# Performance work log

Measured on AMD Instinct MI355X. Metric: run time of the kernel, lower is better.

## Reference

```python
import jax, jax.numpy as jnp
import numpy as np

EPS = 1e-6
NUM_HEADS = 8
FOCUS = 3.0


def setup_inputs() -> dict:
    key = jax.random.key(0)
    ks = jax.random.split(key, 8)
    B, N, C = 16, 4096, 256
    head_dim, ksz = C // NUM_HEADS, 5
    s = 1.0 / np.sqrt(C)
    return {
        "x": jax.random.normal(ks[0], (B, N, C), jnp.float32),
        "Wq": jax.random.normal(ks[1], (C, C), jnp.float32) * s,
        "Wkv": jax.random.normal(ks[2], (C, 2 * C), jnp.float32) * s,
        "Wp": jax.random.normal(ks[3], (C, C), jnp.float32) * s,
        "bp": jnp.zeros((C,), jnp.float32),
        "scale_param": jnp.zeros((1, 1, C), jnp.float32),
        "pos_enc": jax.random.normal(ks[4], (1, N, C), jnp.float32) * 0.02,
        "dwc_w": jax.random.normal(ks[5], (head_dim, 1, ksz, ksz), jnp.float32) * 0.1,
        "dwc_b": jnp.zeros((head_dim,), jnp.float32),
        "H": 64,
        "W": 64,
    }


def _focus(t, scale, f):
    # relu feature map + power focusing with norm restoration
    t = (jax.nn.relu(t) + EPS) / scale
    tn = jnp.linalg.norm(t, axis=-1, keepdims=True)
    tf = t ** f
    return tf / jnp.linalg.norm(tf, axis=-1, keepdims=True) * tn


def reference(x, Wq, Wkv, Wp, bp, scale_param, pos_enc, dwc_w, dwc_b, H, W):
    B, N, C = x.shape
    h = NUM_HEADS
    d = C // h
    n = N  # sr_ratio == 1

    q = x @ Wq                                  # [B,N,C]
    kv = x @ Wkv                                # [B,N,2C]
    k, v = kv[..., :C], kv[..., C:]
    k = k + pos_enc

    scale = jax.nn.softplus(scale_param)
    q = _focus(q, scale, FOCUS)
    k = _focus(k, scale, FOCUS)

    # split heads: [B,h,N,d]
    qh = q.reshape(B, N, h, d).transpose(0, 2, 1, 3)
    kh = k.reshape(B, n, h, d).transpose(0, 2, 1, 3)
    vh = v.reshape(B, n, h, d).transpose(0, 2, 1, 3)

    # linear attention: z = 1/(q . mean_n(k)), kv = k^T v / n, out = (q @ kv) * z
    z = 1.0 / (jnp.einsum("bhnd,bhd->bhn", qh, kh.mean(axis=2)) + EPS)
    kvmat = jnp.einsum("bhnd,bhne->bhde", kh, vh) / n     # [B,h,d,d]
    out = jnp.einsum("bhnd,bhde->bhne", qh, kvmat) * z[..., None]

    out = out.transpose(0, 2, 1, 3).reshape(B, N, C)      # [B,N,C]

    # depthwise conv on v over the HxW grid, per head-channel
    v4 = vh.reshape(B * h, H, W, d).transpose(0, 3, 1, 2)  # [B*h,d,H,W]
    conv = jax.lax.conv_general_dilated(
        v4, dwc_w, window_strides=(1, 1), padding="SAME",
        feature_group_count=d,
        dimension_numbers=("NCHW", "OIHW", "NCHW"))
    conv = conv + dwc_b[None, :, None, None]
    out = out + conv.reshape(B, C, N).transpose(0, 2, 1)

    return out @ Wp + bp
```

## Files before the change

### kernel.cpp

```cpp
#include <hip/hip_runtime.h>
#include <hip/hip_bf16.h>

typedef unsigned short u16;
using bf16_t = __hip_bfloat16;
typedef short short8 __attribute__((ext_vector_type(8)));
typedef float f32x4 __attribute__((ext_vector_type(4)));

__device__ __forceinline__ float b2f(u16 u) {
    return __uint_as_float((unsigned int)u << 16);
}
__device__ __forceinline__ u16 f2b(float f) {
    bf16_t h = __float2bfloat16(f);
    union { bf16_t h; u16 u; } cv; cv.h = h; return cv.u;
}
__device__ __forceinline__ float ldv(const void* p, size_t i, int f32) {
    return f32 ? ((const float*)p)[i] : b2f(((const u16*)p)[i]);
}
__device__ __forceinline__ uint4 pack8(float4 a, float4 b) {
    uint4 u;
    u.x = (unsigned)f2b(a.x) | ((unsigned)f2b(a.y) << 16);
    u.y = (unsigned)f2b(a.z) | ((unsigned)f2b(a.w) << 16);
    u.z = (unsigned)f2b(b.x) | ((unsigned)f2b(b.y) << 16);
    u.w = (unsigned)f2b(b.z) | ((unsigned)f2b(b.w) << 16);
    return u;
}
__device__ __forceinline__ int swz(int n, int k) {
    return k ^ ((n & 7) << 3);
}
__device__ __forceinline__ void gl16(const u16* g, u16* l) {
    __builtin_amdgcn_global_load_lds(
        (const __attribute__((address_space(1))) unsigned int*)g,
        (__attribute__((address_space(3))) unsigned int*)l, 16, 0, 0);
}

__global__ void detect_kernel(const void* __restrict__ x, int* __restrict__ flag)
{
    const int t = threadIdx.x;
    const u16 h = ((const u16*)x)[2 * t];
    const int e = (h >> 7) & 0xFF;
    const int plaus = (e >= 112 && e <= 133) ? 1 : 0;
    const unsigned long long m = __ballot(plaus);
    if (t == 0) flag[0] = (__popcll(m) < 32) ? 1 : 0;
}

__global__ __launch_bounds__(256)
void xcvt_kernel(const void* __restrict__ x, u16* __restrict__ xb,
                 const int* __restrict__ flagp)
{
    const size_t i = ((size_t)blockIdx.x * 256 + threadIdx.x) * 8;
    if (*flagp) {
        const float* xf = (const float*)x + i;
        const float4 f0 = *reinterpret_cast<const float4*>(xf);
        const float4 f1 = *reinterpret_cast<const float4*>(xf + 4);
        *reinterpret_cast<uint4*>(xb + i) = pack8(f0, f1);
    } else {
        *reinterpret_cast<uint4*>(xb + i) =
            *reinterpret_cast<const uint4*>((const u16*)x + i);
    }
}

__global__ __launch_bounds__(256)
void pecvt_kernel(const void* __restrict__ pe, u16* __restrict__ peb,
                  const int* __restrict__ flagp)
{
    const size_t i = ((size_t)blockIdx.x * 256 + threadIdx.x) * 4;
    if (*flagp) {
        const float4 f = *reinterpret_cast<const float4*>((const float*)pe + i);
        ushort4 o; o.x = f2b(f.x); o.y = f2b(f.y); o.z = f2b(f.z); o.w = f2b(f.w);
        *reinterpret_cast<ushort4*>(peb + i) = o;
    } else {
        *reinterpret_cast<ushort4*>(peb + i) =
            *reinterpret_cast<const ushort4*>((const u16*)pe + i);
    }
}

__global__ __launch_bounds__(256)
void wtrans_kernel(const void* __restrict__ W, u16* __restrict__ WT, int N,
                   const int* __restrict__ flagp)
{
    const int f32 = *flagp;
    __shared__ float tile[32][33];
    const int tx = threadIdx.x & 31, ty = threadIdx.x >> 5;
    const int bx = blockIdx.x % (N >> 5);
    const int by = blockIdx.x / (N >> 5);
    #pragma unroll
    for (int r = 0; r < 4; ++r) {
        const int k = by * 32 + ty + r * 8;
        const int n = bx * 32 + tx;
        tile[ty + r * 8][tx] = ldv(W, (size_t)k * N + n, f32);
    }
    __syncthreads();
    #pragma unroll
    for (int r = 0; r < 4; ++r) {
        const int n2 = bx * 32 + ty + r * 8;
        const int k2 = by * 32 + tx;
        WT[(size_t)n2 * 256 + k2] = f2b(tile[tx][ty + r * 8]);
    }
}

template<int MODE>
__global__ __launch_bounds__(256, 2)
void gemm256(const void* __restrict__ Aany, const u16* __restrict__ Abf,
             const u16* __restrict__ BT, u16* __restrict__ O0,
             const void* __restrict__ extra, const int* __restrict__ flagp,
             int abf)
{
    const int f32 = *flagp;
    __shared__ u16 As[128 * 64];
    __shared__ u16 Bs[256 * 64];
    __shared__ float red2[2][128];
    __shared__ float red6[2][128];
    __shared__ float ratio_s[128];
    __shared__ float sscr[256];

    const int tid  = threadIdx.x;
    const int row0 = blockIdx.x * 128;
    const int lane = tid & 63;
    const int wv   = tid >> 6;
    const int wvu  = __builtin_amdgcn_readfirstlane(wv);
    const int wm   = (wv & 1) * 64;
    const int wn   = (wv >> 1) * 128;
    const int l15  = lane & 15;
    const int lq   = lane >> 4;
    const int lr8  = lane >> 3;
    const int lc8  = (lane & 7) * 8;

    if (MODE == 3) {
        const float p = ldv(extra, tid, f32);
        const float s = (p > 20.f) ? p : log1pf(expf(p));
        sscr[tid] = 1.0f / s;
    }

    f32x4 acc[4][8] = {};

    for (int k0 = 0; k0 < 256; k0 += 64) {
        #pragma unroll
        for (int it = 0; it < 8; ++it) {
            const int r = wvu * 64 + it * 8 + lr8;
            gl16(BT + (size_t)r * 256 + k0 + swz(r, lc8),
                 &Bs[(wvu * 64 + it * 8) * 64]);
        }
        if (MODE == 2 || abf || !f32) {
            const u16* Ab = (MODE == 2) ? Abf : (const u16*)Aany;
            #pragma unroll
            for (int it = 0; it < 4; ++it) {
                const int r = wvu * 32 + it * 8 + lr8;
                gl16(Ab + (size_t)(row0 + r) * 256 + k0 + swz(r, lc8),
                     &As[(wvu * 32 + it * 8) * 64]);
            }
        } else {
            const int sr = tid >> 1;
            const int sk = (tid & 1) * 32;
            const float* ag = (const float*)Aany +
                              (size_t)(row0 + sr) * 256 + k0 + sk;
            #pragma unroll
            for (int j = 0; j < 4; ++j) {
                const float4 f0 = *reinterpret_cast<const float4*>(ag + j * 8);
                const float4 f1 = *reinterpret_cast<const float4*>(ag + j * 8 + 4);
                *reinterpret_cast<uint4*>(
                    &As[sr * 64 + swz(sr, sk + j * 8)]) = pack8(f0, f1);
            }
        }
        __syncthreads();
        #pragma unroll
        for (int ks = 0; ks < 64; ks += 32) {
            const int ko = ks + lq * 8;
            short8 av[4], bv[8];
            #pragma unroll
            for (int i = 0; i < 4; ++i) {
                const int m = wm + i * 16 + l15;
                av[i] = *reinterpret_cast<const short8*>(&As[m * 64 + swz(m, ko)]);
            }
            #pragma unroll
            for (int j = 0; j < 8; ++j) {
                const int n = wn + j * 16 + l15;
                bv[j] = *reinterpret_cast<const short8*>(&Bs[n * 64 + swz(n, ko)]);
            }
            #pragma unroll
            for (int i = 0; i < 4; ++i)
                #pragma unroll
                for (int j = 0; j < 8; ++j)
                    acc[i][j] = __builtin_amdgcn_mfma_f32_16x16x32_bf16(
                        av[i], bv[j], acc[i][j], 0, 0, 0);
        }
        __syncthreads();
    }

    if (MODE == 3) {
        #pragma unroll
        for (int i = 0; i < 4; ++i) {
            #pragma unroll
            for (int rg = 0; rg < 4; ++rg) {
                const int lr = wm + i * 16 + lq * 4 + rg;
                float s2 = 0.f, s6 = 0.f;
                #pragma unroll
                for (int j = 0; j < 8; ++j) {
                    const int col = wn + j * 16 + l15;
                    const float xv =
                        (fmaxf(acc[i][j][rg], 0.f) + 1e-6f) * sscr[col];
                    acc[i][j][rg] = xv;
                    const float x2 = xv * xv;
                    s2 += x2;
                    s6 += x2 * x2 * x2;
                }
                #pragma unroll
                for (int off = 1; off < 16; off <<= 1) {
                    s2 += __shfl_xor(s2, off);
                    s6 += __shfl_xor(s6, off);
                }
                if (l15 == 0) { red2[wv >> 1][lr] = s2; red6[wv >> 1][lr] = s6; }
            }
        }
        __syncthreads();
        if (tid < 128)
            ratio_s[tid] = sqrtf((red2[0][tid] + red2[1][tid]) /
                                 (red6[0][tid] + red6[1][tid]));
        __syncthreads();
    }

    #pragma unroll
    for (int i = 0; i < 4; ++i) {
        #pragma unroll
        for (int j = 0; j < 8; ++j) {
            const int gcol = wn + j * 16 + l15;
            #pragma unroll
            for (int rg = 0; rg < 4; ++rg) {
                const int lr = wm + i * 16 + lq * 4 + rg;
                const size_t oi = (size_t)(row0 + lr) * 256 + gcol;
                const float a = acc[i][j][rg];
                if (MODE == 0) {
                    O0[oi] = f2b(a);
                } else if (MODE == 3) {
                    O0[oi] = f2b(a * a * a * ratio_s[lr]);
                } else {
                    const float o = a + ldv(extra, gcol, f32);
                    if (f32) ((float*)O0)[oi] = o;
                    else     O0[oi] = f2b(o);
                }
            }
        }
    }
}

__global__ __launch_bounds__(256, 2)
void fusedk_kernel(const void* __restrict__ x, const u16* __restrict__ WkvT,
                   const u16* __restrict__ peb, const u16* __restrict__ v,
                   const void* __restrict__ sp,
                   float* __restrict__ kvsm, float* __restrict__ ksm,
                   const int* __restrict__ flagp, int abf)
{
    const int f32 = *flagp;
    __shared__ u16 smem[32768];
    __shared__ float red2[4][64];
    __shared__ float red6[4][64];
    __shared__ float ratio_s[64];
    __shared__ float sscr[256];
    u16* As  = smem;
    u16* Bs  = smem + 8192;
    u16* KsT = smem;
    u16* VsT = smem + 16384;

    const int tid  = threadIdx.x;
    const int lane = tid & 63;
    const int wv   = tid >> 6;
    const int wvu  = __builtin_amdgcn_readfirstlane(wv);
    const int l15  = lane & 15;
    const int lq   = lane >> 4;
    const int wn   = wv * 64;
    const int lr8  = lane >> 3;
    const int lc8  = (lane & 7) * 8;

    {
        const float p = ldv(sp, tid, f32);
        const float s = (p > 20.f) ? p : log1pf(expf(p));
        sscr[tid] = 1.0f / s;
    }

    f32x4 cc[2][4] = {};
    float ksp[4] = {0.f, 0.f, 0.f, 0.f};

    const int b    = blockIdx.x >> 5;
    const int row0 = blockIdx.x * 128;
    const int vr   = lane;
    const int veb  = wv * 64;

    f32x4 acc[2][4][4] = {};
    for (int k0 = 0; k0 < 256; k0 += 64) {
        #pragma unroll
        for (int it = 0; it < 8; ++it) {
            const int r = wvu * 64 + it * 8 + lr8;
            gl16(WkvT + (size_t)r * 256 + k0 + swz(r, lc8),
                 &Bs[(wvu * 64 + it * 8) * 64]);
        }
        if (abf || !f32) {
            #pragma unroll
            for (int it = 0; it < 4; ++it) {
                const int r = wvu * 32 + it * 8 + lr8;
                gl16((const u16*)x + (size_t)(row0 + r) * 256 + k0 + swz(r, lc8),
                     &As[(wvu * 32 + it * 8) * 64]);
            }
        } else {
            const int sr = tid >> 1;
            const int sk = (tid & 1) * 32;
            const float* ag = (const float*)x +
                              (size_t)(row0 + sr) * 256 + k0 + sk;
            #pragma unroll
            for (int j = 0; j < 4; ++j) {
                const float4 f0 = *reinterpret_cast<const float4*>(ag + j * 8);
                const float4 f1 = *reinterpret_cast<const float4*>(ag + j * 8 + 4);
                *reinterpret_cast<uint4*>(
                    &As[sr * 64 + swz(sr, sk + j * 8)]) = pack8(f0, f1);
            }
        }
        __syncthreads();
        #pragma unroll
        for (int c = 0; c < 2; ++c) {
            #pragma unroll
            for (int ks = 0; ks < 64; ks += 32) {
                const int ko = ks + lq * 8;
                short8 av[4], bvv[4];
                #pragma unroll
                for (int i = 0; i < 4; ++i) {
                    const int m = c * 64 + i * 16 + l15;
                    av[i] = *reinterpret_cast<const short8*>(&As[m * 64 + swz(m, ko)]);
                }
                #pragma unroll
                for (int j = 0; j < 4; ++j) {
                    const int n = wn + j * 16 + l15;
                    bvv[j] = *reinterpret_cast<const short8*>(&Bs[n * 64 + swz(n, ko)]);
                }
                #pragma unroll
                for (int i = 0; i < 4; ++i)
                    #pragma unroll
                    for (int j = 0; j < 4; ++j)
                        acc[c][i][j] = __builtin_amdgcn_mfma_f32_16x16x32_bf16(
                            av[i], bvv[j], acc[c][i][j], 0, 0, 0);
            }
        }
        __syncthreads();
    }

    #pragma unroll
    for (int c = 0; c < 2; ++c) {
        const int nb = (row0 & 4095) + c * 64;

        #pragma unroll
        for (int i = 0; i < 4; ++i) {
            #pragma unroll
            for (int rg = 0; rg < 4; ++rg) {
                const int lrow = i * 16 + lq * 4 + rg;
                float s2 = 0.f, s6 = 0.f;
                #pragma unroll
                for (int j = 0; j < 4; ++j) {
                    const int col = wn + j * 16 + l15;
                    const float t = acc[c][i][j][rg] +
                        b2f(peb[(size_t)(nb + lrow) * 256 + col]);
                    const float xv = (fmaxf(t, 0.f) + 1e-6f) * sscr[col];
                    acc[c][i][j][rg] = xv;
                    const float x2 = xv * xv;
                    s2 += x2;
                    s6 += x2 * x2 * x2;
                }
                #pragma unroll
                for (int off = 1; off < 16; off <<= 1) {
                    s2 += __shfl_xor(s2, off);
                    s6 += __shfl_xor(s6, off);
                }
                if (l15 == 0) { red2[wv][lrow] = s2; red6[wv][lrow] = s6; }
            }
        }
        __syncthreads();
        if (tid < 64) {
            const float s2t = red2[0][tid] + red2[1][tid] + red2[2][tid] + red2[3][tid];
            const float s6t = red6[0][tid] + red6[1][tid] + red6[2][tid] + red6[3][tid];
            ratio_s[tid] = sqrtf(s2t / s6t);
        }
        __syncthreads();

        {
            float kscol[4] = {0.f, 0.f, 0.f, 0.f};
            #pragma unroll
            for (int i = 0; i < 4; ++i)
                #pragma unroll
                for (int rg = 0; rg < 4; ++rg) {
                    const int lrow = i * 16 + lq * 4 + rg;
                    const float rt = ratio_s[lrow];
                    #pragma unroll
                    for (int j = 0; j < 4; ++j) {
                        const float xv = acc[c][i][j][rg];
                        const float kf = xv * xv * xv * rt;
                        const int d = wn + j * 16 + l15;
                        KsT[d * 64 + swz(d, lrow)] = f2b(kf);
                        kscol[j] += kf;
                    }
                }
            #pragma unroll
            for (int j = 0; j < 4; ++j) {
                float kp = kscol[j];
                kp += __shfl_xor(kp, 16);
                kp += __shfl_xor(kp, 32);
                ksp[j] += kp;
            }
        }

        {
            const u16* vg = v + (size_t)(row0 + c * 64 + vr) * 256 + veb;
            uint4 t0[8];
            #pragma unroll
            for (int j = 0; j < 8; ++j)
                t0[j] = *reinterpret_cast<const uint4*>(vg + j * 8);
            #pragma unroll
            for (int j = 0; j < 8; ++j) {
                const u16* pp = (const u16*)&t0[j];
                #pragma unroll
                for (int m = 0; m < 8; ++m) {
                    const int e = veb + j * 8 + m;
                    VsT[e * 64 + swz(e, vr)] = pp[m];
                }
            }
        }
        __syncthreads();

        #pragma unroll
        for (int hh = 0; hh < 2; ++hh) {
            const int cb = (wv * 2 + hh) * 32;
            const int da = cb + l15, dbx = cb + 16 + l15;
            #pragma unroll
            for (int kk = 0; kk < 64; kk += 32) {
                const int ko = kk + lq * 8;
                const short8 a0 = *reinterpret_cast<const short8*>(
                    &KsT[da * 64 + swz(da, ko)]);
                const short8 a1 = *reinterpret_cast<const short8*>(
                    &KsT[dbx * 64 + swz(dbx, ko)]);
                const short8 b0 = *reinterpret_cast<const short8*>(
                    &VsT[da * 64 + swz(da, ko)]);
                const short8 b1 = *reinterpret_cast<const short8*>(
                    &VsT[dbx * 64 + swz(dbx, ko)]);
                cc[hh][0] = __builtin_amdgcn_mfma_f32_16x16x32_bf16(a0, b0, cc[hh][0], 0, 0, 0);
                cc[hh][1] = __builtin_amdgcn_mfma_f32_16x16x32_bf16(a0, b1, cc[hh][1], 0, 0, 0);
                cc[hh][2] = __builtin_amdgcn_mfma_f32_16x16x32_bf16(a1, b0, cc[hh][2], 0, 0, 0);
                cc[hh][3] = __builtin_amdgcn_mfma_f32_16x16x32_bf16(a1, b1, cc[hh][3], 0, 0, 0);
            }
        }
        __syncthreads();
    }

    const int slot = blockIdx.x & 1;
    float* ksb = ksm + (size_t)(slot * 16 + b) * 256;
    #pragma unroll
    for (int j = 0; j < 4; ++j)
        if (lane < 16)
            atomicAdd(&ksb[wn + j * 16 + lane], ksp[j]);
    #pragma unroll
    for (int hh = 0; hh < 2; ++hh) {
        const int h = wv * 2 + hh;
        float* base = kvsm + ((size_t)(slot * 16 + b) * 8 + h) * 1024;
        #pragma unroll
        for (int rg = 0; rg < 4; ++rg) {
            const int d0 = lq * 4 + rg;
            atomicAdd(&base[(size_t)d0 * 32 + l15],             cc[hh][0][rg]);
            atomicAdd(&base[(size_t)d0 * 32 + 16 + l15],        cc[hh][1][rg]);
            atomicAdd(&base[(size_t)(d0 + 16) * 32 + l15],      cc[hh][2][rg]);
            atomicAdd(&base[(size_t)(d0 + 16) * 32 + 16 + l15], cc[hh][3][rg]);
        }
    }
}

__global__ __launch_bounds__(256, 2)
void attn_mfma_kernel(u16* __restrict__ qy, const float* __restrict__ kvsum,
                      const float* __restrict__ ksum)
{
    __shared__ u16 qs[64 * 256];
    __shared__ u16 kvT[8 * 32 * 40];
    __shared__ float km[8][32];
    __shared__ float zds[64][8];
    const int tid  = threadIdx.x;
    const int lane = tid & 63;
    const int wv   = tid >> 6;
    const int wvu  = __builtin_amdgcn_readfirstlane(wv);
    const int l15  = lane & 15;
    const int lq   = lane >> 4;
    const int b    = blockIdx.x >> 6;
    const int n0   = (blockIdx.x & 63) * 64;
    const float inv_n = 1.0f / 4096.0f;

    {
        const int qr2 = lane >> 5;
        const int qc8 = (lane & 31) * 8;
        const u16* qb = qy + (size_t)(b * 4096 + n0) * 256;
        #pragma unroll
        for (int it = 0; it < 8; ++it) {
            const int r = wvu * 16 + it * 2 + qr2;
            gl16(qb + (size_t)r * 256 + (qc8 ^ ((r & 7) << 3)),
                 &qs[(wvu * 16 + it * 2) * 256]);
        }
    }
    {
        const int h = tid >> 5, e = tid & 31;
        const float* k0 = kvsum + (size_t)b * 8192 + h * 1024 + e;
        const float* k1 = kvsum + (size_t)(16 + b) * 8192 + h * 1024 + e;
        #pragma unroll
        for (int d = 0; d < 32; ++d)
            kvT[h * 1280 + e * 40 + d] = f2b((k0[d * 32] + k1[d * 32]) * inv_n);
        (&km[0][0])[tid] = (ksum[(size_t)b * 256 + tid] +
                            ksum[(size_t)(16 + b) * 256 + tid]) * inv_n;
    }
    __syncthreads();

    {
        const int zt = tid & 63;
        const int zh0 = (tid >> 6) * 2;
        #pragma unroll
        for (int hh = 0; hh < 2; ++hh) {
            const int h = zh0 + hh;
            float s = 0.f;
            #pragma unroll
            for (int d = 0; d < 32; ++d) {
                const int col = (h * 32 + d) ^ ((zt & 7) << 3);
                s = fmaf(b2f(qs[zt * 256 + col]), km[h][d], s);
            }
            zds[zt][h] = s;
        }
    }

    f32x4 acc[8][2];
    #pragma unroll
    for (int h = 0; h < 8; ++h) {
        const int m = wvu * 16 + l15;
        const int col = (h * 32 + lq * 8) ^ ((m & 7) << 3);
        const short8 av = *reinterpret_cast<const short8*>(&qs[m * 256 + col]);
        const short8 b0 = *reinterpret_cast<const short8*>(
            &kvT[h * 1280 + l15 * 40 + lq * 8]);
        const short8 b1 = *reinterpret_cast<const short8*>(
            &kvT[h * 1280 + (16 + l15) * 40 + lq * 8]);
        const f32x4 z = {0.f, 0.f, 0.f, 0.f};
        acc[h][0] = __builtin_amdgcn_mfma_f32_16x16x32_bf16(av, b0, z, 0, 0, 0);
        acc[h][1] = __builtin_amdgcn_mfma_f32_16x16x32_bf16(av, b1, z, 0, 0, 0);
    }
    __syncthreads();

    u16* qb = qy + (size_t)(b * 4096 + n0) * 256;
    #pragma unroll
    for (int h = 0; h < 8; ++h) {
        #pragma unroll
        for (int eh = 0; eh < 2; ++eh) {
            const int gcol = h * 32 + eh * 16 + l15;
            #pragma unroll
            for (int rg = 0; rg < 4; ++rg) {
                const int lr = wvu * 16 + lq * 4 + rg;
                const float z = 1.0f / (zds[lr][h] + 1e-6f);
                qb[(size_t)lr * 256 + gcol] = f2b(acc[h][eh][rg] * z);
            }
        }
    }
}

__global__ __launch_bounds__(256, 2)
void conv_add_kernel(const u16* __restrict__ v, const void* __restrict__ w,
                     const void* __restrict__ bias, u16* __restrict__ y,
                     const int* __restrict__ flagp)
{
    const int f32 = *flagp;
    __shared__ u16 vt[144 * 256];
    __shared__ float wl[800];
    __shared__ float bl[32];
    const int tid = threadIdx.x;
    for (int i = tid; i < 800; i += 256) wl[i] = ldv(w, i, f32);
    if (tid < 32) bl[tid] = ldv(bias, tid, f32);

    const int bb = blockIdx.x >> 6;
    const int ty = (blockIdx.x >> 3) & 7;
    const int tx = blockIdx.x & 7;
    const int y0 = ty * 8, x0 = tx * 8;
    const u16* vb = v + (size_t)bb * 4096 * 256;

    #pragma unroll
    for (int it = 0; it < 18; ++it) {
        const int idx = it * 256 + tid;
        const int px  = idx >> 5;
        const int c8  = (idx & 31) * 8;
        const int py  = px / 12, pxx = px - py * 12;
        const int yy = y0 + py - 2, xx = x0 + pxx - 2;
        uint4 val = {0u, 0u, 0u, 0u};
        if (yy >= 0 && yy < 64 && xx >= 0 && xx < 64)
            val = *reinterpret_cast<const uint4*>(
                vb + (size_t)((yy << 6) + xx) * 256 + c8);
        *reinterpret_cast<uint4*>(&vt[px * 256 + c8]) = val;
    }
    __syncthreads();

    const int c  = tid;
    const int dc = c & 31;
    float wreg[25];
    #pragma unroll
    for (int i = 0; i < 25; ++i) wreg[i] = wl[dc * 25 + i];
    const float bv = bl[dc];

    float win[5][12];
    #pragma unroll
    for (int r = 0; r < 5; ++r)
        #pragma unroll
        for (int cc = 0; cc < 12; ++cc)
            win[r][cc] = b2f(vt[(r * 12 + cc) * 256 + c]);

    u16* yb = y + ((size_t)bb * 4096 + (size_t)y0 * 64 + x0) * 256 + c;
    #pragma unroll
    for (int oy = 0; oy < 8; ++oy) {
        if (oy) {
            #pragma unroll
            for (int r = 0; r < 4; ++r)
                #pragma unroll
                for (int cc = 0; cc < 12; ++cc) win[r][cc] = win[r + 1][cc];
            #pragma unroll
            for (int cc = 0; cc < 12; ++cc)
                win[4][cc] = b2f(vt[((oy + 4) * 12 + cc) * 256 + c]);
        }
        #pragma unroll
        for (int ox = 0; ox < 8; ++ox) {
            float s = 0.f;
            #pragma unroll
            for (int ky = 0; ky < 5; ++ky)
                #pragma unroll
                for (int kx = 0; kx < 5; ++kx)
                    s = fmaf(win[ky][ox + kx], wreg[ky * 5 + kx], s);
            u16* yp = yb + (size_t)(oy * 64 + ox) * 256;
            *yp = f2b(b2f(*yp) + s + bv);
        }
    }
}

extern "C" void kernel_launch(void* const* d_in, const int* in_sizes, int n_in,
                              void* d_out, int out_size, void* d_ws, size_t ws_size,
                              hipStream_t stream)
{
    (void)in_sizes; (void)n_in; (void)out_size;
    const void* x   = d_in[0];
    const void* Wq  = d_in[1];
    const void* Wkv = d_in[2];
    const void* Wp  = d_in[3];
    const void* bp  = d_in[4];
    const void* sp  = d_in[5];
    const void* pe  = d_in[6];
    const void* dw  = d_in[7];
    const void* db  = d_in[8];

    int*   flag = (int*)d_ws;
    float* kvsm = (float*)((char*)d_ws + 64);
    float* ksm  = kvsm + 262144;
    u16*   WqT  = (u16*)(ksm + 8192);
    u16*   WkvT = WqT + 65536;
    u16*   WpT  = WkvT + 131072;
    u16*   peb  = WpT + 65536;
    u16*   qy   = peb + 1048576;
    u16*   xb   = qy + (size_t)16777216;
    u16*   v    = (u16*)d_out;

    const size_t need = (size_t)((char*)(xb + 16777216) - (char*)d_ws);
    const int big = (ws_size >= need) ? 1 : 0;

    hipMemsetAsync(kvsm, 0, (262144 + 8192) * sizeof(float), stream);
    detect_kernel<<<1, 64, 0, stream>>>(x, flag);
    if (big) xcvt_kernel<<<8192, 256, 0, stream>>>(x, xb, flag);
    pecvt_kernel<<<1024, 256, 0, stream>>>(pe, peb, flag);
    wtrans_kernel<<<64, 256, 0, stream>>>(Wq, WqT, 256, flag);
    wtrans_kernel<<<128, 256, 0, stream>>>(Wkv, WkvT, 512, flag);
    wtrans_kernel<<<64, 256, 0, stream>>>(Wp, WpT, 256, flag);

    const void* Ax = big ? (const void*)xb : x;

    hipLaunchKernelGGL((gemm256<3>), dim3(512), dim3(256), 0, stream,
                       Ax, (const u16*)nullptr, WqT, qy, sp, flag, big);
    hipLaunchKernelGGL((gemm256<0>), dim3(512), dim3(256), 0, stream,
                       Ax, (const u16*)nullptr, WkvT + (size_t)256 * 256, v,
                       (const void*)nullptr, flag, big);
    fusedk_kernel<<<512, 256, 0, stream>>>(Ax, WkvT, peb, v, sp, kvsm, ksm,
                                           flag, big);

    attn_mfma_kernel<<<1024, 256, 0, stream>>>(qy, kvsm, ksm);
    conv_add_kernel<<<1024, 256, 0, stream>>>(v, dw, db, qy, flag);
    hipLaunchKernelGGL((gemm256<2>), dim3(512), dim3(256), 0, stream,
                       (const void*)nullptr, qy, WpT, (u16*)d_out, bp, flag, 0);
}
```

Baseline: 325.5 us.

## Merge prep kernels and halve V staging LDS in fused k kernel

The pe conversion and three weight-transpose kernels are merged into one launch with block-index dispatch, cutting three launches. In the fused k/kv kernel, V is now staged into shared memory in two 128-column halves, with one head per wave per pass, so the smem buffer shrinks from 32768 to 24576 u16. The smaller LDS footprint may allow more resident blocks, at the cost of an extra pair of barriers per chunk. The head mapping for the atomics is updated to match, and a no-op ternary is added in the conv index.

```diff
diff --git a/kernel.cpp b/kernel.cpp
--- a/kernel.cpp
+++ b/kernel.cpp
@@ -60,29 +60,35 @@
 }
 
 __global__ __launch_bounds__(256)
-void pecvt_kernel(const void* __restrict__ pe, u16* __restrict__ peb,
-                  const int* __restrict__ flagp)
-{
-    const size_t i = ((size_t)blockIdx.x * 256 + threadIdx.x) * 4;
-    if (*flagp) {
-        const float4 f = *reinterpret_cast<const float4*>((const float*)pe + i);
-        ushort4 o; o.x = f2b(f.x); o.y = f2b(f.y); o.z = f2b(f.z); o.w = f2b(f.w);
-        *reinterpret_cast<ushort4*>(peb + i) = o;
-    } else {
-        *reinterpret_cast<ushort4*>(peb + i) =
-            *reinterpret_cast<const ushort4*>((const u16*)pe + i);
-    }
-}
-
-__global__ __launch_bounds__(256)
-void wtrans_kernel(const void* __restrict__ W, u16* __restrict__ WT, int N,
-                   const int* __restrict__ flagp)
+void prep_kernel(const void* __restrict__ pe, u16* __restrict__ peb,
+                 const void* __restrict__ Wq, u16* __restrict__ WqT,
+                 const void* __restrict__ Wkv, u16* __restrict__ WkvT,
+                 const void* __restrict__ Wp, u16* __restrict__ WpT,
+                 const int* __restrict__ flagp)
 {
     const int f32 = *flagp;
     __shared__ float tile[32][33];
+    const int bid = blockIdx.x;
+    if (bid < 1024) {
+        const size_t i = ((size_t)bid * 256 + threadIdx.x) * 4;
+        if (f32) {
+            const float4 f = *reinterpret_cast<const float4*>((const float*)pe + i);
+            ushort4 o; o.x = f2b(f.x); o.y = f2b(f.y); o.z = f2b(f.z); o.w = f2b(f.w);
+            *reinterpret_cast<ushort4*>(peb + i) = o;
+        } else {
+            *reinterpret_cast<ushort4*>(peb + i) =
+                *reinterpret_cast<const ushort4*>((const u16*)pe + i);
+        }
+        return;
+    }
+    int lb = bid - 1024;
+    const void* W; u16* WT; int N;
+    if (lb < 64)       { W = Wq;  WT = WqT;  N = 256; }
+    else if (lb < 192) { W = Wkv; WT = WkvT; N = 512; lb -= 64; }
+    else               { W = Wp;  WT = WpT;  N = 256; lb -= 192; }
     const int tx = threadIdx.x & 31, ty = threadIdx.x >> 5;
-    const int bx = blockIdx.x % (N >> 5);
-    const int by = blockIdx.x / (N >> 5);
+    const int bx = lb % (N >> 5);
+    const int by = lb / (N >> 5);
     #pragma unroll
     for (int r = 0; r < 4; ++r) {
         const int k = by * 32 + ty + r * 8;
@@ -250,7 +256,7 @@
                    const int* __restrict__ flagp, int abf)
 {
     const int f32 = *flagp;
-    __shared__ u16 smem[32768];
+    __shared__ u16 smem[24576];
     __shared__ float red2[4][64];
     __shared__ float red6[4][64];
     __shared__ float ratio_s[64];
@@ -281,8 +287,6 @@
 
     const int b    = blockIdx.x >> 5;
     const int row0 = blockIdx.x * 128;
-    const int vr   = lane;
-    const int veb  = wv * 64;
 
     f32x4 acc[2][4][4] = {};
     for (int k0 = 0; k0 < 256; k0 += 64) {
@@ -403,46 +407,49 @@
             }
         }
 
-        {
-            const u16* vg = v + (size_t)(row0 + c * 64 + vr) * 256 + veb;
-            uint4 t0[8];
-            #pragma unroll
-            for (int j = 0; j < 8; ++j)
-                t0[j] = *reinterpret_cast<const uint4*>(vg + j * 8);
-            #pragma unroll
-            for (int j = 0; j < 8; ++j) {
-                const u16* pp = (const u16*)&t0[j];
-                #pragma unroll
-                for (int m = 0; m < 8; ++m) {
-                    const int e = veb + j * 8 + m;
-                    VsT[e * 64 + swz(e, vr)] = pp[m];
-                }
-            }
-        }
-        __syncthreads();
-
-        #pragma unroll
-        for (int hh = 0; hh < 2; ++hh) {
-            const int cb = (wv * 2 + hh) * 32;
-            const int da = cb + l15, dbx = cb + 16 + l15;
-            #pragma unroll
-            for (int kk = 0; kk < 64; kk += 32) {
-                const int ko = kk + lq * 8;
-                const short8 a0 = *reinterpret_cast<const short8*>(
-                    &KsT[da * 64 + swz(da, ko)]);
-                const short8 a1 = *reinterpret_cast<const short8*>(
-                    &KsT[dbx * 64 + swz(dbx, ko)]);
-                const short8 b0 = *reinterpret_cast<const short8*>(
-                    &VsT[da * 64 + swz(da, ko)]);
-                const short8 b1 = *reinterpret_cast<const short8*>(
-                    &VsT[dbx * 64 + swz(dbx, ko)]);
-                cc[hh][0] = __builtin_amdgcn_mfma_f32_16x16x32_bf16(a0, b0, cc[hh][0], 0, 0, 0);
-                cc[hh][1] = __builtin_amdgcn_mfma_f32_16x16x32_bf16(a0, b1, cc[hh][1], 0, 0, 0);
-                cc[hh][2] = __builtin_amdgcn_mfma_f32_16x16x32_bf16(a1, b0, cc[hh][2], 0, 0, 0);
-                cc[hh][3] = __builtin_amdgcn_mfma_f32_16x16x32_bf16(a1, b1, cc[hh][3], 0, 0, 0);
-            }
-        }
-        __syncthreads();
+        #pragma unroll
+        for (int p = 0; p < 2; ++p) {
+            {
+                const u16* vg = v + (size_t)(row0 + c * 64 + lane) * 256 +
+                                p * 128 + wv * 32;
+                uint4 t0[4];
+                #pragma unroll
+                for (int j = 0; j < 4; ++j)
+                    t0[j] = *reinterpret_cast<const uint4*>(vg + j * 8);
+                #pragma unroll
+                for (int j = 0; j < 4; ++j) {
+                    const u16* pp = (const u16*)&t0[j];
+                    #pragma unroll
+                    for (int m = 0; m < 8; ++m) {
+                        const int el = wv * 32 + j * 8 + m;
+                        VsT[el * 64 + swz(el, lane)] = pp[m];
+                    }
+                }
+            }
+            __syncthreads();
+            {
+                const int h  = p * 4 + wv;
+                const int cb = h * 32;
+                const int el = wv * 32;
+                #pragma unroll
+                for (int kk = 0; kk < 64; kk += 32) {
+                    const int ko = kk + lq * 8;
+                    const short8 a0 = *reinterpret_cast<const short8*>(
+                        &KsT[(cb + l15) * 64 + swz(cb + l15, ko)]);
+                    const short8 a1 = *reinterpret_cast<const short8*>(
+                        &KsT[(cb + 16 + l15) * 64 + swz(cb + 16 + l15, ko)]);
+                    const short8 b0 = *reinterpret_cast<const short8*>(
+                        &VsT[(el + l15) * 64 + swz(el + l15, ko)]);
+                    const short8 b1 = *reinterpret_cast<const short8*>(
+                        &VsT[(el + 16 + l15) * 64 + swz(el + 16 + l15, ko)]);
+                    cc[p][0] = __builtin_amdgcn_mfma_f32_16x16x32_bf16(a0, b0, cc[p][0], 0, 0, 0);
+                    cc[p][1] = __builtin_amdgcn_mfma_f32_16x16x32_bf16(a0, b1, cc[p][1], 0, 0, 0);
+                    cc[p][2] = __builtin_amdgcn_mfma_f32_16x16x32_bf16(a1, b0, cc[p][2], 0, 0, 0);
+                    cc[p][3] = __builtin_amdgcn_mfma_f32_16x16x32_bf16(a1, b1, cc[p][3], 0, 0, 0);
+                }
+            }
+            __syncthreads();
+        }
     }
 
     const int slot = blockIdx.x & 1;
@@ -453,7 +460,7 @@
             atomicAdd(&ksb[wn + j * 16 + lane], ksp[j]);
     #pragma unroll
     for (int hh = 0; hh < 2; ++hh) {
-        const int h = wv * 2 + hh;
+        const int h = hh * 4 + wv;
         float* base = kvsm + ((size_t)(slot * 16 + b) * 8 + h) * 1024;
         #pragma unroll
         for (int rg = 0; rg < 4; ++rg) {
@@ -622,7 +629,7 @@
             for (int ky = 0; ky < 5; ++ky)
                 #pragma unroll
                 for (int kx = 0; kx < 5; ++kx)
-                    s = fmaf(win[ky][ox + kx], wreg[ky * 5 + kx], s);
+                    s = fmaf(win[oy ? ky : ky][ox + kx], wreg[ky * 5 + kx], s);
             u16* yp = yb + (size_t)(oy * 64 + ox) * 256;
             *yp = f2b(b2f(*yp) + s + bv);
         }
@@ -661,10 +668,8 @@
     hipMemsetAsync(kvsm, 0, (262144 + 8192) * sizeof(float), stream);
     detect_kernel<<<1, 64, 0, stream>>>(x, flag);
     if (big) xcvt_kernel<<<8192, 256, 0, stream>>>(x, xb, flag);
-    pecvt_kernel<<<1024, 256, 0, stream>>>(pe, peb, flag);
-    wtrans_kernel<<<64, 256, 0, stream>>>(Wq, WqT, 256, flag);
-    wtrans_kernel<<<128, 256, 0, stream>>>(Wkv, WkvT, 512, flag);
-    wtrans_kernel<<<64, 256, 0, stream>>>(Wp, WpT, 256, flag);
+    prep_kernel<<<1280, 256, 0, stream>>>(pe, peb, Wq, WqT, Wkv, WkvT,
+                                          Wp, WpT, flag);
 
     const void* Ax = big ? (const void*)xb : x;
 
```

Measured after the change: 312.2 us. 4.1% less time.
